# Performance work log

Hardware: AMD Instinct MI355X
Metric: run time of the kernel (lower is better)

The kernel has to match this reference:

```python
import jax, jax.numpy as jnp
import numpy as np
from jax import lax

S, T = 128, 32768            # seq_len (tokens), token_size (samples per token)
K, STRIDE = 1024, 512        # kernel/fourier size, stride
HE, HD, C = 1024, 1024, 1024 # enc_hidden, dec_hidden, output classes
NW = (T - K) // STRIDE + 1   # 63 windows per token

_WIN_IDX = np.arange(NW)[:, None] * STRIDE + np.arange(K)  # (NW, K)

def strided_fourier(x):
    # x: (..., T) -> real part of FFT over each strided window: (..., NW, K)
    w = x[..., _WIN_IDX]
    return jnp.fft.fft(w, axis=-1).real.astype(x.dtype)

def _lstm_cell(h, c, gates, H):
    # torch gate order: i, f, g, o
    i = jax.nn.sigmoid(gates[..., 0:H])
    f = jax.nn.sigmoid(gates[..., H:2 * H])
    g = jnp.tanh(gates[..., 2 * H:3 * H])
    o = jax.nn.sigmoid(gates[..., 3 * H:4 * H])
    c = f * c + i * g
    h = o * jnp.tanh(c)
    return h, c


def setup_inputs() -> dict:
    key = jax.random.key(0)
    ks = jax.random.split(key, 13)
    def n(k, shape, s=0.02):
        return (jax.random.normal(k, shape, jnp.float32) * s)
    return {
        "x": jax.random.normal(ks[0], (S, T), jnp.float32),
        "Wih_e": n(ks[1], (4 * HE, K)), "Whh_e": n(ks[2], (4 * HE, HE)), "b_e": n(ks[3], (4 * HE,)),
        "Wm1": n(ks[4], (HE, HE)), "bm1": n(ks[5], (HE,)),
        "Wm2": n(ks[6], (HD, HE)), "bm2": n(ks[7], (HD,)),
        "Wih_d": n(ks[8], (4 * HD, K)), "Whh_d": n(ks[9], (4 * HD, HD)), "b_d": n(ks[10], (4 * HD,)),
        "Wo": n(ks[11], (C, HD)), "bo": n(ks[12], (C,)),
    }


def reference(x, Wih_e, Whh_e, b_e, Wm1, bm1, Wm2, bm2, Wih_d, Whh_d, b_d, Wo, bo):
    # --- strided FFT features (dropout=0 -> identity) ---
    fouriers = strided_fourier(x)  # (S, NW, K)

    # --- encoder LSTM: batch=S, time=NW ---
    def enc_step(carry, xt):  # xt: (S, K)
        h, c = carry
        gates = xt @ Wih_e.T + h @ Whh_e.T + b_e
        return _lstm_cell(h, c, gates, HE), None
    z = jnp.zeros((S, HE), x.dtype)
    (h_enc, _), _ = lax.scan(enc_step, (z, z), jnp.swapaxes(fouriers, 0, 1))

    # --- mid linear on final hidden: Linear->ReLU->Linear->Tanh ---
    h_mid = jnp.tanh(jax.nn.relu(h_enc @ Wm1.T + bm1) @ Wm2.T + bm2)  # (S, HD)
    h0 = h_mid[0]  # (HD,); torch code uses h for both h and c init

    # --- decoder: sequential over tokens, hidden carried across steps ---
    def outer(carry, fw):  # fw: (NW, K)
        def inner(hc, xt):  # xt: (K,)
            h, c = hc
            gates = xt @ Wih_d.T + h @ Whh_d.T + b_d
            return _lstm_cell(h, c, gates, HD), None
        (h, c), _ = lax.scan(inner, carry, fw)
        # dec_output[-1] == final hidden h
        out = jax.nn.log_softmax(h @ Wo.T + bo, axis=0)  # (C,)
        return (h, c), out

    _, outputs = lax.scan(outer, (h0, h0), fouriers)
    return outputs  # (S, C)
```

## Files before the change

### kernel.cpp

```cpp
#include <hip/hip_runtime.h>

typedef unsigned short u16;
typedef unsigned u32;
typedef unsigned long long u64;
typedef __bf16 bf16x8 __attribute__((ext_vector_type(8)));
typedef _Float16 half8 __attribute__((ext_vector_type(8)));
typedef _Float16 half2v __attribute__((ext_vector_type(2)));
typedef float f32x4 __attribute__((ext_vector_type(4)));
typedef unsigned uint4v __attribute__((ext_vector_type(4)));
typedef unsigned uint2v __attribute__((ext_vector_type(2)));

__device__ __forceinline__ u16 f2b(float f) {
  unsigned u = __builtin_bit_cast(unsigned, f);
  u = (u + 0x7FFFu + ((u >> 16) & 1u)) >> 16;
  return (u16)u;
}
__device__ __forceinline__ float b2f(u16 h) {
  return __builtin_bit_cast(float, ((unsigned)h) << 16);
}
__device__ __forceinline__ u16 f2h(float f) {
  _Float16 h = (_Float16)f;
  return __builtin_bit_cast(unsigned short, h);
}
__device__ __forceinline__ float sigmoidf_(float x) { return 1.0f / (1.0f + expf(-x)); }
__device__ __forceinline__ float fsig(float x) {
  x = fminf(fmaxf(x, -30.f), 30.f);
  return 1.0f / (1.0f + __expf(-x));
}
__device__ __forceinline__ float ftanh_(float x) {
  x = fminf(fmaxf(x, -15.f), 15.f);
  float e = __expf(2.0f * x);
  return (e - 1.0f) / (e + 1.0f);
}
__device__ __forceinline__ u64 aload(const u64* p) {
  return __hip_atomic_load(p, __ATOMIC_RELAXED, __HIP_MEMORY_SCOPE_AGENT);
}

__device__ __forceinline__ float fdot2_(u32 a, u32 b, float c) {
#if __has_builtin(__builtin_amdgcn_fdot2)
  return __builtin_amdgcn_fdot2(__builtin_bit_cast(half2v, a),
                                __builtin_bit_cast(half2v, b), c, false);
#else
  half2v x = __builtin_bit_cast(half2v, a), y = __builtin_bit_cast(half2v, b);
  return c + (float)x.x * (float)y.x + (float)x.y * (float)y.y;
#endif
}

__device__ __forceinline__ u64 l2_load1(const u64* p) {
  uint2v r;
  asm volatile("global_load_dwordx2 %0, %1, off sc0\n\ts_waitcnt vmcnt(0)"
               : "=&v"(r) : "v"(p) : "memory");
  return ((u64)r.y << 32) | (u64)r.x;
}
__device__ __forceinline__ void l2_store(u64* p, u64 v) {
  asm volatile("global_store_dwordx2 %0, %1, off sc0" :: "v"(p), "v"(v) : "memory");
}

template <int EPI, bool OUTBF, bool ACC, bool SLAB = false>
__global__ __launch_bounds__(256) void gemm_bt(
    const u16* __restrict__ A, int lda,
    const u16* __restrict__ B, int ldb,
    void* __restrict__ Cout, int ldc,
    const float* __restrict__ bias,
    int M, int N, int K) {
  __shared__ __align__(16) u16 As[64 * 40];
  __shared__ __align__(16) u16 Bs[64 * 40];
  const int t = threadIdx.x;
  const int n0 = blockIdx.x * 64, m0 = blockIdx.y * 64;
  const int wave = t >> 6, lane = t & 63;
  const int wm = (wave >> 1) * 32, wn = (wave & 1) * 32;
  const int quad = lane >> 4, r16 = lane & 15;
  const int srow = t >> 2, scol = (t & 3) * 8;
  f32x4 acc[2][2] = {};
  const u16* ap = A + (size_t)(m0 + srow) * lda + scol;
  const u16* bp = B + (size_t)(n0 + srow) * ldb + scol;
  for (int k0 = 0; k0 < K; k0 += 32) {
    uint4 av = *(const uint4*)(ap + k0);
    uint4 bv = *(const uint4*)(bp + k0);
    __syncthreads();
    *(uint4*)&As[srow * 40 + scol] = av;
    *(uint4*)&Bs[srow * 40 + scol] = bv;
    __syncthreads();
    bf16x8 a0 = *(const bf16x8*)&As[(wm + r16) * 40 + quad * 8];
    bf16x8 a1 = *(const bf16x8*)&As[(wm + 16 + r16) * 40 + quad * 8];
    bf16x8 b0 = *(const bf16x8*)&Bs[(wn + r16) * 40 + quad * 8];
    bf16x8 b1 = *(const bf16x8*)&Bs[(wn + 16 + r16) * 40 + quad * 8];
    acc[0][0] = __builtin_amdgcn_mfma_f32_16x16x32_bf16(a0, b0, acc[0][0], 0, 0, 0);
    acc[0][1] = __builtin_amdgcn_mfma_f32_16x16x32_bf16(a0, b1, acc[0][1], 0, 0, 0);
    acc[1][0] = __builtin_amdgcn_mfma_f32_16x16x32_bf16(a1, b0, acc[1][0], 0, 0, 0);
    acc[1][1] = __builtin_amdgcn_mfma_f32_16x16x32_bf16(a1, b1, acc[1][1], 0, 0, 0);
  }
  for (int mi = 0; mi < 2; mi++)
    for (int ni = 0; ni < 2; ni++)
      for (int r = 0; r < 4; r++) {
        int gm = m0 + wm + mi * 16 + quad * 4 + r;
        int gn = n0 + wn + ni * 16 + r16;
        float v = acc[mi][ni][r];
        size_t idx;
        if (SLAB) {
          int q = gn >> 10, bb = (gn >> 5) & 31, jj = gn & 31;
          idx = ((size_t)bb * 8064 + gm) * 128 + q * 32 + jj;
        } else {
          idx = (size_t)gm * ldc + gn;
        }
        if (ACC) v += ((float*)Cout)[idx];
        if (bias) v += bias[gn];
        if (EPI == 1) v = fmaxf(v, 0.0f);
        if (EPI == 2) v = tanhf(v);
        if (OUTBF) ((u16*)Cout)[idx] = f2b(v);
        else ((float*)Cout)[idx] = v;
      }
}

__global__ __launch_bounds__(256) void k_cos(u16* __restrict__ Chi, u16* __restrict__ Clo) {
  int gid = blockIdx.x * 256 + threadIdx.x;
  int k = gid >> 10, n = gid & 1023;
  int m = (k * n) & 1023;
  float c = cospif((float)m * (1.0f / 512.0f));
  u16 hi = f2b(c);
  Chi[gid] = hi;
  Clo[gid] = f2b(c - b2f(hi));
}

__global__ __launch_bounds__(256) void k_win(const float* __restrict__ x,
                                             u16* __restrict__ Whi, u16* __restrict__ Wlo) {
  int gid = blockIdx.x * 256 + threadIdx.x;
  int e = gid * 4;
  int r = e >> 10, n = e & 1023;
  int wI = r >> 7, s = r & 127;
  const float* src = x + (size_t)s * 32768 + wI * 512 + n;
  float4 v = *(const float4*)src;
  float vv[4] = {v.x, v.y, v.z, v.w};
#pragma unroll
  for (int i = 0; i < 4; i++) {
    u16 hi = f2b(vv[i]);
    Whi[e + i] = hi;
    Wlo[e + i] = f2b(vv[i] - b2f(hi));
  }
}

__global__ __launch_bounds__(256) void k_f2bk(const float* __restrict__ src, u16* __restrict__ dst) {
  int gid = blockIdx.x * 256 + threadIdx.x;
  int i = gid * 4;
  float4 v = *(const float4*)(src + i);
  dst[i] = f2b(v.x); dst[i + 1] = f2b(v.y); dst[i + 2] = f2b(v.z); dst[i + 3] = f2b(v.w);
}

__global__ __launch_bounds__(256) void k_perm(const u16* __restrict__ F1, u16* __restrict__ F2) {
  int gid = blockIdx.x * 256 + threadIdx.x;
  int ro = gid >> 7, n8 = (gid & 127) * 8;
  int s = ro / 63, wI = ro % 63;
  *(uint4*)&F2[(size_t)ro * 1024 + n8] = *(const uint4*)&F1[(size_t)(wI * 128 + s) * 1024 + n8];
}

__global__ __launch_bounds__(256) void k_cell_enc(const float* __restrict__ g,
                                                  const u16* __restrict__ gihe, int t0,
                                                  float* __restrict__ c_e,
                                                  u16* __restrict__ At) {
  int gid = blockIdx.x * 256 + threadIdx.x;
  int s = gid >> 10, j = gid & 1023;
  const float* gr = g + (size_t)s * 4096;
  const u16* er = gihe + (size_t)(t0 * 128 + s) * 4096;
  float iv = sigmoidf_(gr[j] + b2f(er[j]));
  float fv = sigmoidf_(gr[j + 1024] + b2f(er[j + 1024]));
  float gv = tanhf(gr[j + 2048] + b2f(er[j + 2048]));
  float ov = sigmoidf_(gr[j + 3072] + b2f(er[j + 3072]));
  float c = fv * c_e[gid] + iv * gv;
  c_e[gid] = c;
  At[(size_t)s * 1024 + j] = f2b(ov * tanhf(c));
}

__global__ void k_initdec(const float* __restrict__ hmid, u64* __restrict__ hb,
                          int* __restrict__ ctrl, u64* __restrict__ probe,
                          u32* __restrict__ verdict) {
  int gid = blockIdx.x * blockDim.x + threadIdx.x;
  if (gid < 512) {
    u32 lo = (u32)f2h(hmid[2 * gid]) | ((u32)f2h(hmid[2 * gid + 1]) << 16);
    hb[gid] = (u64)lo;
  } else if (gid < 1024) {
    hb[gid] = 0xFFFFFFFF00000000ull;
  }
  if (gid < 9) ctrl[gid] = (gid == 8) ? -1 : 0;
  if (gid >= 16 && gid < 48) probe[gid - 16] = 0ull;
  if (gid >= 48 && gid < 80) verdict[gid - 48] = 0u;
}

__global__ __launch_bounds__(512, 2) void dec_persist(
    const float* __restrict__ Whh, const u16* __restrict__ GihS,
    const float* __restrict__ hmid,
    u64* __restrict__ hb, float* __restrict__ hfinal,
    int* __restrict__ ctrl, u64* __restrict__ probe, u32* __restrict__ verdict) {
  const int t = threadIdx.x;
  u32 xcd = __builtin_amdgcn_s_getreg(63508) & 7u;
  __shared__ int sslot;
  if (t == 0) {
    int tk = atomicAdd(&ctrl[xcd], 1);
    if (tk == 31) atomicCAS(&ctrl[8], -1, (int)xcd);
    int ch;
    do {
      ch = __hip_atomic_load(&ctrl[8], __ATOMIC_RELAXED, __HIP_MEMORY_SCOPE_AGENT);
    } while (ch < 0);
    sslot = (xcd == (u32)ch && tk < 32) ? tk : -1;
  }
  __syncthreads();
  const int b = sslot;
  if (b < 0) return;

  __shared__ int sok;
  if (t == 0) sok = 1;
  __syncthreads();
  for (int r = 0; r < 8; r++) {
    if (sok) {
      if (t == 0) l2_store(&probe[b], (u64)(0xC0DE0000u + (u32)r));
      if (t < 32) {
        const u64 want = (u64)(0xC0DE0000u + (u32)r);
        bool got = false;
        int lim = (r == 0) ? 30000 : 4000;
        for (int it = 0; it < lim; it++) {
          if (l2_load1(&probe[t]) >= want) { got = true; break; }
        }
        if (!got) sok = 0;
      }
    }
    __syncthreads();
  }
  if (t == 0)
    __hip_atomic_store(&verdict[b], sok ? 2u : 1u, __ATOMIC_RELAXED, __HIP_MEMORY_SCOPE_AGENT);
  __shared__ int modef;
  if (t == 0) modef = 2;
  __syncthreads();
  if (t < 32) {
    u32 v;
    do {
      v = __hip_atomic_load(&verdict[t], __ATOMIC_RELAXED, __HIP_MEMORY_SCOPE_AGENT);
    } while (v == 0);
    if (v != 2) atomicMin(&modef, 1);
  }
  __syncthreads();
  const bool fast = (modef == 2);

  const int w = t >> 6, lane = t & 63;
  const int quad = lane >> 4, r16 = lane & 15;
  const int hh = lane >> 5, jj = lane & 31;

  half8 afrag[2][4];
#pragma unroll
  for (int mt = 0; mt < 2; mt++) {
    int lr = mt * 16 + r16;
    const float* Wr = Whh + (size_t)(b * 32 + lr) * 1024 + 128 * w + quad * 8;
#pragma unroll
    for (int ks = 0; ks < 4; ks++) {
      half8 v;
#pragma unroll
      for (int j = 0; j < 8; j++) v[j] = (_Float16)Wr[ks * 32 + j];
      afrag[mt][ks] = v;
    }
  }
  u32 wv[3][32];
#pragma unroll
  for (int j = 0; j < 3; j++) {
    const float* Wr = Whh + (size_t)((j + 1) * 1024 + b * 32 + jj) * 1024 + 128 * w + 64 * hh;
#pragma unroll
    for (int i = 0; i < 16; i++) {
      float4 f = *(const float4*)(Wr + 4 * i);
      wv[j][2 * i]     = (u32)f2h(f.x) | ((u32)f2h(f.y) << 16);
      wv[j][2 * i + 1] = (u32)f2h(f.z) | ((u32)f2h(f.w) << 16);
    }
  }

  __shared__ __align__(16) u32 hsu[512];
  __shared__ __align__(16) float gpart[2][8][128];
  __shared__ __align__(16) u16 uslab[2][2048];

  {
    uint2v g0 = *(const uint2v*)(GihS + (size_t)b * 8064 * 128 + t * 4);
    *(uint2v*)&uslab[0][t * 4] = g0;
  }
  float cst = (t < 32) ? hmid[b * 32 + t] : 0.0f;

  int n = 0;
  for (int s = 0; s < 128; s++) {
    for (int wI = 0; wI < 63; wI++, n++) {
      const u32 tn = (u32)n;
      const u64* p = hb + (size_t)(n & 1) * 512 + t;
      u64 v;
      if (fast) {
        do { v = l2_load1(p); } while ((u32)(v >> 32) != tn);
      } else {
        for (;;) {
          v = aload(p);
          if ((u32)(v >> 32) == tn) break;
        }
      }
      hsu[t] = (u32)v;

      const bool slabload = (n & 15) == 0;
      uint2v gsv;
      if (slabload) {
        int nn = (n + 16 <= 8048) ? n + 16 : 8048;
        gsv = *(const uint2v*)(GihS + ((size_t)b * 8064 + nn) * 128 + t * 4);
      }

      f32x4 acc0 = {0.f, 0.f, 0.f, 0.f}, acc1 = {0.f, 0.f, 0.f, 0.f};
      float accV[3] = {0.f, 0.f, 0.f};
#pragma unroll
      for (int g = 0; g < 4; g++) {
        half8 bfv = *(const half8*)&hsu[64 * w + 16 * g + 4 * quad];
        uint4v h0 = *(const uint4v*)&hsu[64 * w + 32 * hh + 8 * g];
        uint4v h1 = *(const uint4v*)&hsu[64 * w + 32 * hh + 8 * g + 4];
        acc0 = __builtin_amdgcn_mfma_f32_16x16x32_f16(afrag[0][g], bfv, acc0, 0, 0, 0);
        acc1 = __builtin_amdgcn_mfma_f32_16x16x32_f16(afrag[1][g], bfv, acc1, 0, 0, 0);
#pragma unroll
        for (int i2 = 0; i2 < 4; i2++)
#pragma unroll
          for (int j = 0; j < 3; j++)
            accV[j] = fdot2_(wv[j][8 * g + i2], h0[i2], accV[j]);
#pragma unroll
        for (int i2 = 0; i2 < 4; i2++)
#pragma unroll
          for (int j = 0; j < 3; j++)
            accV[j] = fdot2_(wv[j][8 * g + 4 + i2], h1[i2], accV[j]);
      }
      const int pb = n & 1;
      if (r16 == 0) {
        *(f32x4*)&gpart[pb][w][4 * quad] = acc0;
        *(f32x4*)&gpart[pb][w][16 + 4 * quad] = acc1;
      }
#pragma unroll
      for (int j = 0; j < 3; j++) {
        float sum = accV[j] + __shfl_xor(accV[j], 32);
        if (lane < 32) gpart[pb][w][32 + jj + 32 * j] = sum;
      }
      __syncthreads();
      if (slabload) *(uint2v*)&uslab[((n >> 4) + 1) & 1][t * 4] = gsv;
      if (w == 0) {
        const int sb = (n >> 4) & 1, so = (n & 15) * 128;
        const int rA = lane, rB = 64 + lane;
        float sA = 0.f, sB = 0.f;
#pragma unroll
        for (int ww = 0; ww < 8; ww++) {
          sA += gpart[pb][ww][rA];
          sB += gpart[pb][ww][rB];
        }
        sA += b2f(uslab[sb][so + rA]);
        sB += b2f(uslab[sb][so + rB]);
        float gA = fsig(sA);
        float gB = (lane < 32) ? ftanh_(sB) : fsig(sB);
        float fx = __shfl_xor(gA, 32);
        float ox = __shfl_xor(gB, 32);
        if (lane < 32) {
          cst = fx * cst + gA * gB;
          float h = ox * ftanh_(cst);
          u32 h16 = (u32)f2h(h);
          u32 oth = (u32)__shfl_down((int)h16, 1);
          if ((lane & 1) == 0) {
            u64 word = ((u64)(u32)(n + 1) << 32) | (h16 | (oth << 16));
            u64* dst = &hb[(size_t)((n + 1) & 1) * 512 + b * 16 + (lane >> 1)];
            if (fast) l2_store(dst, word);
            else __hip_atomic_store(dst, word, __ATOMIC_RELAXED, __HIP_MEMORY_SCOPE_AGENT);
          }
          if (wI == 62) hfinal[(size_t)s * 1024 + b * 32 + lane] = h;
        }
      }
    }
  }
}

__global__ __launch_bounds__(256) void k_lsm(const float* __restrict__ logits, float* __restrict__ out) {
  int s = blockIdx.x, t = threadIdx.x;
  const float* L = logits + (size_t)s * 1024;
  __shared__ float red[4], red2[4];
  float m = -1e30f;
  for (int i = t; i < 1024; i += 256) m = fmaxf(m, L[i]);
  for (int o = 1; o < 64; o <<= 1) m = fmaxf(m, __shfl_xor(m, o));
  if ((t & 63) == 0) red[t >> 6] = m;
  __syncthreads();
  m = fmaxf(fmaxf(red[0], red[1]), fmaxf(red[2], red[3]));
  float sum = 0.f;
  for (int i = t; i < 1024; i += 256) sum += expf(L[i] - m);
  for (int o = 1; o < 64; o <<= 1) sum += __shfl_xor(sum, o);
  if ((t & 63) == 0) red2[t >> 6] = sum;
  __syncthreads();
  sum = red2[0] + red2[1] + red2[2] + red2[3];
  float lse = m + logf(sum);
  for (int i = t; i < 1024; i += 256) out[(size_t)s * 1024 + i] = L[i] - lse;
}

extern "C" void kernel_launch(void* const* d_in, const int* in_sizes, int n_in,
                              void* d_out, int out_size, void* d_ws, size_t ws_size,
                              hipStream_t stream) {
  const float* x     = (const float*)d_in[0];
  const float* Wih_e = (const float*)d_in[1];
  const float* Whh_e = (const float*)d_in[2];
  const float* b_e   = (const float*)d_in[3];
  const float* Wm1   = (const float*)d_in[4];
  const float* bm1   = (const float*)d_in[5];
  const float* Wm2   = (const float*)d_in[6];
  const float* bm2   = (const float*)d_in[7];
  const float* Wih_d = (const float*)d_in[8];
  const float* Whh_d = (const float*)d_in[9];
  const float* b_d   = (const float*)d_in[10];
  const float* Wo    = (const float*)d_in[11];
  const float* bo    = (const float*)d_in[12];
  float* out = (float*)d_out;

  char* w = (char*)d_ws;
  size_t off = 0;
  auto alloc = [&](size_t bytes) { size_t r = off; off += (bytes + 255) & ~(size_t)255; return r; };
  u16* Chi = (u16*)(w + alloc((size_t)1024 * 1024 * 2));
  u16* Clo = (u16*)(w + alloc((size_t)1024 * 1024 * 2));
  u16* F1  = (u16*)(w + alloc((size_t)8064 * 1024 * 2));
  char* f2slot = w + alloc((size_t)8064 * 1024 * 2);
  u16* WinHi = (u16*)f2slot;
  u16* F2    = (u16*)f2slot;
  u16* WinLo = (u16*)(w + alloc((size_t)8064 * 1024 * 2));
  char* gislot = w + alloc((size_t)8064 * 4096 * 2);
  float* Fgem = (float*)gislot;
  u16* GihS   = (u16*)gislot;
  u16* Gihe = (u16*)(w + alloc((size_t)8064 * 4096 * 2));
  u16* Wihd  = (u16*)(w + alloc((size_t)4096 * 1024 * 2));
  u16* Wihe  = (u16*)(w + alloc((size_t)4096 * 1024 * 2));
  u16* Whhe  = (u16*)(w + alloc((size_t)4096 * 1024 * 2));
  u16* Wm1b = (u16*)(w + alloc((size_t)1024 * 1024 * 2));
  u16* Wm2b = (u16*)(w + alloc((size_t)1024 * 1024 * 2));
  u16* Wob  = (u16*)(w + alloc((size_t)1024 * 1024 * 2));
  u16* At   = (u16*)(w + alloc((size_t)128 * 1024 * 2));
  float* Ge = (float*)(w + alloc((size_t)128 * 4096 * 4));
  float* Ce = (float*)(w + alloc((size_t)128 * 1024 * 4));
  u16* Mid1 = (u16*)(w + alloc((size_t)128 * 1024 * 2));
  float* Hmid = (float*)(w + alloc((size_t)128 * 1024 * 4));
  u64* Hb = (u64*)(w + alloc((size_t)1024 * 8));
  int* Ctrl = (int*)(w + alloc(256));
  u64* Probe = (u64*)(w + alloc(256));
  u32* Verdict = (u32*)(w + alloc(256));
  float* Hfin = (float*)(w + alloc((size_t)128 * 1024 * 4));
  u16* Hfinb  = (u16*)(w + alloc((size_t)128 * 1024 * 2));
  float* Logit = (float*)(w + alloc((size_t)128 * 1024 * 4));
  (void)ws_size; (void)in_sizes; (void)n_in; (void)out_size;

  hipMemsetAsync(At, 0, (size_t)128 * 1024 * 2, stream);
  hipMemsetAsync(Ce, 0, (size_t)128 * 1024 * 4, stream);

  k_cos<<<4096, 256, 0, stream>>>(Chi, Clo);
  k_win<<<8064, 256, 0, stream>>>(x, WinHi, WinLo);
  gemm_bt<0, false, false><<<dim3(16, 126), 256, 0, stream>>>(WinHi, 1024, Chi, 1024, Fgem, 1024, nullptr, 8064, 1024, 1024);
  gemm_bt<0, false, true><<<dim3(16, 126), 256, 0, stream>>>(WinHi, 1024, Clo, 1024, Fgem, 1024, nullptr, 8064, 1024, 1024);
  gemm_bt<0, false, true><<<dim3(16, 126), 256, 0, stream>>>(WinLo, 1024, Chi, 1024, Fgem, 1024, nullptr, 8064, 1024, 1024);
  k_f2bk<<<8064, 256, 0, stream>>>(Fgem, F1);
  k_perm<<<4032, 256, 0, stream>>>(F1, F2);

  k_f2bk<<<4096, 256, 0, stream>>>(Wih_d, Wihd);
  k_f2bk<<<4096, 256, 0, stream>>>(Wih_e, Wihe);
  k_f2bk<<<4096, 256, 0, stream>>>(Whh_e, Whhe);
  k_f2bk<<<1024, 256, 0, stream>>>(Wm1, Wm1b);
  k_f2bk<<<1024, 256, 0, stream>>>(Wm2, Wm2b);
  k_f2bk<<<1024, 256, 0, stream>>>(Wo, Wob);

  gemm_bt<0, true, false, true><<<dim3(64, 126), 256, 0, stream>>>(F2, 1024, Wihd, 1024, GihS, 128, b_d, 8064, 4096, 1024);
  gemm_bt<0, true, false><<<dim3(64, 126), 256, 0, stream>>>(F1, 1024, Wihe, 1024, Gihe, 4096, b_e, 8064, 4096, 1024);

  for (int t = 0; t < 63; t++) {
    gemm_bt<0, false, false><<<dim3(64, 2), 256, 0, stream>>>(At, 1024, Whhe, 1024, Ge, 4096, nullptr, 128, 4096, 1024);
    k_cell_enc<<<512, 256, 0, stream>>>(Ge, Gihe, t, Ce, At);
  }

  gemm_bt<1, true, false><<<dim3(16, 2), 256, 0, stream>>>(At, 1024, Wm1b, 1024, Mid1, 1024, bm1, 128, 1024, 1024);
  gemm_bt<2, false, false><<<dim3(16, 2), 256, 0, stream>>>(Mid1, 1024, Wm2b, 1024, Hmid, 1024, bm2, 128, 1024, 1024);

  k_initdec<<<4, 256, 0, stream>>>(Hmid, Hb, Ctrl, Probe, Verdict);
  dec_persist<<<256, 512, 0, stream>>>(Whh_d, GihS, Hmid, Hb, Hfin, Ctrl, Probe, Verdict);

  k_f2bk<<<128, 256, 0, stream>>>(Hfin, Hfinb);
  gemm_bt<0, false, false><<<dim3(16, 2), 256, 0, stream>>>(Hfinb, 1024, Wob, 1024, Logit, 1024, bo, 128, 1024, 1024);
  k_lsm<<<128, 256, 0, stream>>>(Logit, out);
}
```

Before: 18.08 ms.

## Poll hidden-state flags from one wavefront and relay via LDS flags

In the fast path, only wavefront 7 spins on the global hidden-state buffer, reading 8 tagged entries per lane with wide sc0 loads. It writes the payload into LDS and publishes per-lane release flags. The other wavefronts spin on the LDS flags instead of polling global memory. This cuts L2 polling traffic from all wavefronts, at the cost of an extra LDS hop and a serial dependence on one wavefront's latency.

```diff
diff --git a/kernel.cpp b/kernel.cpp
--- a/kernel.cpp
+++ b/kernel.cpp
@@ -271,28 +271,61 @@
   __shared__ __align__(16) u32 hsu[512];
   __shared__ __align__(16) float gpart[2][8][128];
   __shared__ __align__(16) u16 uslab[2][2048];
-
+  __shared__ u32 flags[64];
+
+  if (t < 64) flags[t] = 0xFFFFFFFFu;
   {
     uint2v g0 = *(const uint2v*)(GihS + (size_t)b * 8064 * 128 + t * 4);
     *(uint2v*)&uslab[0][t * 4] = g0;
   }
   float cst = (t < 32) ? hmid[b * 32 + t] : 0.0f;
+  __syncthreads();
 
   int n = 0;
   for (int s = 0; s < 128; s++) {
     for (int wI = 0; wI < 63; wI++, n++) {
       const u32 tn = (u32)n;
-      const u64* p = hb + (size_t)(n & 1) * 512 + t;
-      u64 v;
       if (fast) {
-        do { v = l2_load1(p); } while ((u32)(v >> 32) != tn);
+        if (w == 7) {
+          const u64* base = hb + (size_t)(n & 1) * 512 + 8 * lane;
+          for (;;) {
+            uint4v r0, r1, r2, r3;
+            asm volatile(
+                "global_load_dwordx4 %0, %4, off sc0\n\t"
+                "global_load_dwordx4 %1, %4, off offset:16 sc0\n\t"
+                "global_load_dwordx4 %2, %4, off offset:32 sc0\n\t"
+                "global_load_dwordx4 %3, %4, off offset:48 sc0\n\t"
+                "s_waitcnt vmcnt(0)"
+                : "=&v"(r0), "=&v"(r1), "=&v"(r2), "=&v"(r3)
+                : "v"(base) : "memory");
+            bool ok = (r0.y == tn) & (r0.w == tn) & (r1.y == tn) & (r1.w == tn) &
+                      (r2.y == tn) & (r2.w == tn) & (r3.y == tn) & (r3.w == tn);
+            if (ok) {
+              uint4v d0 = {r0.x, r0.z, r1.x, r1.z};
+              uint4v d1 = {r2.x, r2.z, r3.x, r3.z};
+              *(uint4v*)&hsu[8 * lane] = d0;
+              *(uint4v*)&hsu[8 * lane + 4] = d1;
+              __hip_atomic_store(&flags[lane], tn, __ATOMIC_RELEASE,
+                                 __HIP_MEMORY_SCOPE_WORKGROUP);
+              break;
+            }
+          }
+        } else {
+          u32 fv;
+          do {
+            fv = __hip_atomic_load(&flags[8 * w + (lane & 7)], __ATOMIC_ACQUIRE,
+                                   __HIP_MEMORY_SCOPE_WORKGROUP);
+          } while (!__all(fv == tn));
+        }
       } else {
+        const u64* p = hb + (size_t)(n & 1) * 512 + t;
+        u64 v;
         for (;;) {
           v = aload(p);
           if ((u32)(v >> 32) == tn) break;
         }
-      }
-      hsu[t] = (u32)v;
+        hsu[t] = (u32)v;
+      }
 
       const bool slabload = (n & 15) == 0;
       uint2v gsv;
```

Measured after the change: 18.14 ms. About the same (+0.3%).
